# Kernel optimization log

Measured on AMD Instinct MI355X. Metric: run time of the kernel, lower is better.

Reference implementation:

```python
import jax, jax.numpy as jnp
import numpy as np

N_NODES = 100000
N_EDGES = 1600000
IN_DIM = 256
HID = 128
ALPHA = 0.1
K_STEPS = 10


def setup_inputs() -> dict:
    key = jax.random.key(0)
    ks = jax.random.split(key, 10)
    x = jax.random.normal(ks[0], (N_NODES, IN_DIM), dtype=jnp.float32)
    edge_index = jax.random.randint(ks[1], (2, N_EDGES), 0, N_NODES, dtype=jnp.int64)
    s = 0.02
    W1 = jax.random.normal(ks[2], (HID, IN_DIM), dtype=jnp.float32) * s
    b1 = jnp.zeros((HID,), dtype=jnp.float32)
    W2 = jax.random.normal(ks[3], (HID, HID), dtype=jnp.float32) * s
    b2 = jnp.zeros((HID,), dtype=jnp.float32)
    W3 = jax.random.normal(ks[4], (HID, HID), dtype=jnp.float32) * s
    b3 = jnp.zeros((HID,), dtype=jnp.float32)
    Wo = jax.random.normal(ks[5], (1, HID), dtype=jnp.float32) * s
    bo = jnp.zeros((1,), dtype=jnp.float32)
    return {"x": x, "edge_index": edge_index, "W1": W1, "b1": b1,
            "W2": W2, "b2": b2, "W3": W3, "b3": b3, "Wo": Wo, "bo": bo}


def _gcn_norm(edge_index, num_nodes):
    # add self-loops, then symmetric normalization 1/sqrt(deg_i * deg_j)
    loop = jnp.arange(num_nodes, dtype=edge_index.dtype)
    src = jnp.concatenate([edge_index[0], loop])
    dst = jnp.concatenate([edge_index[1], loop])
    ones = jnp.ones(src.shape[0], dtype=jnp.float32)
    deg = jax.ops.segment_sum(ones, dst, num_segments=num_nodes)
    dinv = jnp.where(deg > 0, jax.lax.rsqrt(deg), 0.0)
    norm = dinv[src] * dinv[dst]
    return src, dst, norm


def reference(x, edge_index, W1, b1, W2, b2, W3, b3, Wo, bo):
    # MLP encoder (dropout=0 -> identity in eval)
    h = jax.nn.relu(x @ W1.T + b1)
    h = jax.nn.relu(h @ W2.T + b2)
    h = jax.nn.relu(h @ W3.T + b3)
    # APPNP propagation: h <- (1-alpha) * A_hat h + alpha * h0
    n = x.shape[0]
    src, dst, norm = _gcn_norm(edge_index, n)
    h0 = h
    for _ in range(K_STEPS):
        msg = norm[:, None] * h[src]            # [E+N, HID]
        agg = jax.ops.segment_sum(msg, dst, num_segments=n)
        h = (1.0 - ALPHA) * agg + ALPHA * h0
    out = h @ Wo.T + bo                          # [N, 1]
    return out.squeeze(-1)
```

## Files before the change

### kernel.cpp

```cpp
#include <hip/hip_runtime.h>

#define NN   100000
#define NE   1600000
#define IND  256
#define HIDD 128
#define BCAP 64
#define NPART 196
#define SCAP 10240
#define APITCH 40
#define HPITCH 136
#define NGE  1563
#define NFA  782

typedef __attribute__((ext_vector_type(8))) short short8v;
typedef __attribute__((ext_vector_type(4))) float f32x4;

__device__ inline unsigned packbf2(float x, float y) {
  unsigned xb = __float_as_uint(x);
  unsigned yb = __float_as_uint(y);
  xb += 0x7fffu + ((xb >> 16) & 1u);
  yb += 0x7fffu + ((yb >> 16) & 1u);
  return (xb >> 16) | (yb & 0xffff0000u);
}
__device__ inline unsigned short bf16r(float x) {
  unsigned b = __float_as_uint(x);
  b += 0x7fffu + ((b >> 16) & 1u);
  return (unsigned short)(b >> 16);
}

__global__ void wcvt_all(const float* __restrict__ W1, const float* __restrict__ W2,
                         const float* __restrict__ W3, unsigned* __restrict__ W1b,
                         unsigned* __restrict__ W2b, unsigned* __restrict__ W3b) {
  int i = blockIdx.x * 256 + threadIdx.x;
  const float* src; unsigned* dst; int off;
  if (i < 16384)      { src = W1; dst = W1b; off = i; }
  else if (i < 24576) { src = W2; dst = W2b; off = i - 16384; }
  else                { src = W3; dst = W3b; off = i - 24576; }
  float2 v = ((const float2*)src)[off];
  dst[off] = packbf2(v.x, v.y);
}

__global__ __launch_bounds__(256) void enc_fillA(
    const float* __restrict__ x,
    const unsigned short* __restrict__ W1b, const float* __restrict__ b1,
    const unsigned short* __restrict__ W2b, const float* __restrict__ b2,
    const unsigned short* __restrict__ W3b, const float* __restrict__ b3,
    const float* __restrict__ Wo, float* __restrict__ z,
    const int* __restrict__ src, const int* __restrict__ dst,
    int* __restrict__ gcur, unsigned* __restrict__ sbuf)
{
  __shared__ unsigned short hbuf[64 * HPITCH];
  __shared__ float zsh[2][64];
  __shared__ int hist[NPART];
  __shared__ int lofs[NPART];
  const int tid = threadIdx.x;
  const int bid = blockIdx.x;
  const int r3v = bid % 3;

  if (r3v == 2) {
    int fi = bid / 3;
    const int base = fi * 2048;
    for (int i = tid; i < NPART; i += 256) hist[i] = 0;
    __syncthreads();
    int d[8], s[8];
#pragma unroll
    for (int i = 0; i < 8; ++i) {
      int e = base + i * 256 + tid;
      bool v = e < NE;
      d[i] = v ? dst[e] : -1;
      s[i] = v ? src[e] : 0;
      if (v) atomicAdd(&hist[d[i] >> 9], 1);
    }
    __syncthreads();
    for (int i = tid; i < NPART; i += 256)
      lofs[i] = hist[i] ? atomicAdd(&gcur[i], hist[i]) : 0;
    __syncthreads();
#pragma unroll
    for (int i = 0; i < 8; ++i) {
      if (d[i] >= 0) {
        int p = d[i] >> 9;
        int q = atomicAdd(&lofs[p], 1);
        if (q < SCAP)
          sbuf[(size_t)p * SCAP + q] = ((unsigned)(d[i] & 511) << 17) | (unsigned)s[i];
      }
    }
    return;
  }

  const int gb = (bid / 3) * 2 + r3v;
  if (gb >= NGE) return;
  unsigned short* lA = hbuf;
  const int lane = tid & 63, wid = tid >> 6;
  const int wr = wid >> 1, wc = wid & 1;
  const int bm = gb * 64;
  const int lr = lane & 15, lg = lane >> 4;

  f32x4 acc[2][4];
#pragma unroll
  for (int i = 0; i < 2; ++i)
#pragma unroll
    for (int j = 0; j < 4; ++j) acc[i][j] = (f32x4){0.f, 0.f, 0.f, 0.f};

  for (int k0 = 0; k0 < IND; k0 += 32) {
    {
      int rr = tid >> 2, g = tid & 3;
      int grow = bm + rr;
      float4 v0 = make_float4(0.f, 0.f, 0.f, 0.f), v1 = v0;
      if (grow < NN) {
        const float* ap = x + (size_t)grow * IND + k0 + g * 8;
        v0 = ((const float4*)ap)[0]; v1 = ((const float4*)ap)[1];
      }
      uint4 pk;
      pk.x = packbf2(v0.x, v0.y); pk.y = packbf2(v0.z, v0.w);
      pk.z = packbf2(v1.x, v1.y); pk.w = packbf2(v1.z, v1.w);
      *(uint4*)&lA[rr * APITCH + g * 8] = pk;
    }
    __syncthreads();
    {
      short8v a[2], b[4];
#pragma unroll
      for (int i = 0; i < 2; ++i)
        a[i] = *(const short8v*)&lA[(wr * 32 + i * 16 + lr) * APITCH + lg * 8];
#pragma unroll
      for (int j = 0; j < 4; ++j)
        b[j] = *(const short8v*)&W1b[(size_t)(wc * 64 + j * 16 + lr) * IND + k0 + lg * 8];
#pragma unroll
      for (int i = 0; i < 2; ++i)
#pragma unroll
        for (int j = 0; j < 4; ++j)
          acc[i][j] = __builtin_amdgcn_mfma_f32_16x16x32_bf16(a[i], b[j], acc[i][j], 0, 0, 0);
    }
    __syncthreads();
  }
#pragma unroll
  for (int i = 0; i < 2; ++i)
#pragma unroll
    for (int e = 0; e < 4; ++e) {
      int lrow = wr * 32 + i * 16 + lg * 4 + e;
#pragma unroll
      for (int j = 0; j < 4; ++j) {
        int cc = wc * 64 + j * 16 + lr;
        hbuf[lrow * HPITCH + cc] = bf16r(fmaxf(acc[i][j][e] + b1[cc], 0.f));
      }
    }
  __syncthreads();

#pragma unroll
  for (int i = 0; i < 2; ++i)
#pragma unroll
    for (int j = 0; j < 4; ++j) acc[i][j] = (f32x4){0.f, 0.f, 0.f, 0.f};
  for (int k0 = 0; k0 < HIDD; k0 += 32) {
    short8v a[2], b[4];
#pragma unroll
    for (int i = 0; i < 2; ++i)
      a[i] = *(const short8v*)&hbuf[(wr * 32 + i * 16 + lr) * HPITCH + k0 + lg * 8];
#pragma unroll
    for (int j = 0; j < 4; ++j)
      b[j] = *(const short8v*)&W2b[(size_t)(wc * 64 + j * 16 + lr) * HIDD + k0 + lg * 8];
#pragma unroll
    for (int i = 0; i < 2; ++i)
#pragma unroll
      for (int j = 0; j < 4; ++j)
        acc[i][j] = __builtin_amdgcn_mfma_f32_16x16x32_bf16(a[i], b[j], acc[i][j], 0, 0, 0);
  }
  __syncthreads();
#pragma unroll
  for (int i = 0; i < 2; ++i)
#pragma unroll
    for (int e = 0; e < 4; ++e) {
      int lrow = wr * 32 + i * 16 + lg * 4 + e;
#pragma unroll
      for (int j = 0; j < 4; ++j) {
        int cc = wc * 64 + j * 16 + lr;
        hbuf[lrow * HPITCH + cc] = bf16r(fmaxf(acc[i][j][e] + b2[cc], 0.f));
      }
    }
  __syncthreads();

#pragma unroll
  for (int i = 0; i < 2; ++i)
#pragma unroll
    for (int j = 0; j < 4; ++j) acc[i][j] = (f32x4){0.f, 0.f, 0.f, 0.f};
  for (int k0 = 0; k0 < HIDD; k0 += 32) {
    short8v a[2], b[4];
#pragma unroll
    for (int i = 0; i < 2; ++i)
      a[i] = *(const short8v*)&hbuf[(wr * 32 + i * 16 + lr) * HPITCH + k0 + lg * 8];
#pragma unroll
    for (int j = 0; j < 4; ++j)
      b[j] = *(const short8v*)&W3b[(size_t)(wc * 64 + j * 16 + lr) * HIDD + k0 + lg * 8];
#pragma unroll
    for (int i = 0; i < 2; ++i)
#pragma unroll
      for (int j = 0; j < 4; ++j)
        acc[i][j] = __builtin_amdgcn_mfma_f32_16x16x32_bf16(a[i], b[j], acc[i][j], 0, 0, 0);
  }
  float wv[4];
#pragma unroll
  for (int j = 0; j < 4; ++j) wv[j] = Wo[wc * 64 + j * 16 + lr];
  if (tid < 128) { zsh[tid >> 6][tid & 63] = 0.f; }
  __syncthreads();
#pragma unroll
  for (int i = 0; i < 2; ++i)
#pragma unroll
    for (int e = 0; e < 4; ++e) {
      float part = 0.f;
#pragma unroll
      for (int j = 0; j < 4; ++j) {
        int cc = wc * 64 + j * 16 + lr;
        part += fmaxf(acc[i][j][e] + b3[cc], 0.f) * wv[j];
      }
#pragma unroll
      for (int off = 8; off > 0; off >>= 1) part += __shfl_down(part, off, 16);
      if (lr == 0) zsh[wc][wr * 32 + i * 16 + lg * 4 + e] = part;
    }
  __syncthreads();
  if (tid < 64) {
    int row = bm + tid;
    if (row < NN) z[row] = zsh[0][tid] + zsh[1][tid];
  }
}

__global__ __launch_bounds__(256, 8) void fill_phaseB(
    const unsigned* __restrict__ sbuf, const int* __restrict__ gcur,
    const float* __restrict__ z, int* __restrict__ colbuk,
    int* __restrict__ deg, float* __restrict__ dinv, float* __restrict__ va)
{
  __shared__ int lcur[512];
  const int tid = threadIdx.x;
  const int b = blockIdx.x;
  for (int i = tid; i < 512; i += 256) lcur[i] = 0;
  __syncthreads();
  int cnt = min(gcur[b], SCAP);
  const unsigned* sp = sbuf + (size_t)b * SCAP;
  for (int i = tid; i < cnt; i += 256) {
    unsigned u = sp[i];
    int dloc = (int)(u >> 17);
    int s = (int)(u & 0x1FFFFu);
    int pos = atomicAdd(&lcur[dloc], 1);
    if (pos < BCAP) colbuk[(size_t)((b << 9) + dloc) * BCAP + pos] = s;
  }
  __syncthreads();
  for (int i = tid; i < 512; i += 256) {
    int node = (b << 9) + i;
    if (node < NN) {
      int dg = lcur[i];
      float di = rsqrtf((float)(dg + 1));
      deg[node] = dg;
      dinv[node] = di;
      va[node] = di * z[node];
    }
  }
}

template<int LAST>
__global__ __launch_bounds__(256, 8) void appnp_sstep(
    const float* __restrict__ vin, const float* __restrict__ z,
    const float* __restrict__ dinv, const int* __restrict__ deg,
    const int* __restrict__ colbuk, float* __restrict__ vout,
    const float* __restrict__ bo, float* __restrict__ out)
{
  int tid = threadIdx.x;
  int sl = tid & 15;
  int node = blockIdx.x * 16 + (tid >> 4);
  if (node >= NN) return;
  int m = min(deg[node], BCAP);
  float val = (sl == 0) ? vin[node] : 0.f;
  for (int j = sl; j < m; j += 16)
    val += vin[colbuk[(size_t)node * BCAP + j]];
#pragma unroll
  for (int off = 8; off > 0; off >>= 1) val += __shfl_down(val, off, 16);
  if (sl == 0) {
    float di = dinv[node];
    float s = 0.9f * di * val + 0.1f * z[node];
    if (LAST) out[node] = s + bo[0];
    else vout[node] = di * s;
  }
}

extern "C" void kernel_launch(void* const* d_in, const int* in_sizes, int n_in,
                              void* d_out, int out_size, void* d_ws, size_t ws_size,
                              hipStream_t stream) {
  const float* x   = (const float*)d_in[0];
  const int*   ei  = (const int*)d_in[1];
  const float* W1  = (const float*)d_in[2];
  const float* b1  = (const float*)d_in[3];
  const float* W2  = (const float*)d_in[4];
  const float* b2  = (const float*)d_in[5];
  const float* W3  = (const float*)d_in[6];
  const float* b3  = (const float*)d_in[7];
  const float* Wo  = (const float*)d_in[8];
  const float* bo  = (const float*)d_in[9];
  float* out = (float*)d_out;

  const int* srcv = ei;
  const int* dstv = ei + NE;

  int*      colbuk = (int*)d_ws;
  unsigned* sbuf   = (unsigned*)(colbuk + (size_t)NN * BCAP);
  int*      gcur   = (int*)(sbuf + (size_t)NPART * SCAP);
  int*      deg    = gcur + NPART;
  float*    dinv   = (float*)(deg + NN);
  float*    zbuf   = dinv + NN;
  float*    va     = zbuf + NN;
  float*    vb     = va + NN;
  unsigned* W1b    = (unsigned*)(vb + NN);
  unsigned* W2b    = W1b + 16384;
  unsigned* W3b    = W2b + 8192;

  hipMemsetAsync(gcur, 0, NPART * 4, stream);

  wcvt_all<<<128, 256, 0, stream>>>(W1, W2, W3, W1b, W2b, W3b);

  enc_fillA<<<2346, 256, 0, stream>>>(x, (unsigned short*)W1b, b1,
                                      (unsigned short*)W2b, b2,
                                      (unsigned short*)W3b, b3, Wo, zbuf,
                                      srcv, dstv, gcur, sbuf);

  fill_phaseB<<<NPART, 256, 0, stream>>>(sbuf, gcur, zbuf, colbuk, deg, dinv, va);

  int ssb = (NN + 15) / 16;
  float* cur = va; float* nxt = vb;
  for (int k = 0; k < 9; ++k) {
    appnp_sstep<0><<<ssb, 256, 0, stream>>>(cur, zbuf, dinv, deg, colbuk,
                                            nxt, nullptr, nullptr);
    float* t = cur; cur = nxt; nxt = t;
  }
  appnp_sstep<1><<<ssb, 256, 0, stream>>>(cur, zbuf, dinv, deg, colbuk,
                                          nullptr, bo, out);
}
```

Before: 207.6 us.

## Replace fixed-capacity neighbor buckets with compact CSR built via per-block scans

Measured after the change: 220.1 us. 1.06x slower.

```diff
diff --git a/kernel.cpp b/kernel.cpp
--- a/kernel.cpp
+++ b/kernel.cpp
@@ -4,13 +4,11 @@
 #define NE   1600000
 #define IND  256
 #define HIDD 128
-#define BCAP 64
 #define NPART 196
 #define SCAP 10240
 #define APITCH 40
 #define HPITCH 136
 #define NGE  1563
-#define NFA  782
 
 typedef __attribute__((ext_vector_type(8))) short short8v;
 typedef __attribute__((ext_vector_type(4))) float f32x4;
@@ -221,53 +219,91 @@
   }
 }
 
-__global__ __launch_bounds__(256, 8) void fill_phaseB(
+__global__ __launch_bounds__(256) void wscan(const int* __restrict__ gcur,
+                                             int* __restrict__ wbase) {
+  __shared__ int sc[2][256];
+  int t = threadIdx.x;
+  int v = (t < NPART) ? min(gcur[t], SCAP) : 0;
+  sc[0][t] = v;
+  __syncthreads();
+  int pp = 0;
+  for (int off = 1; off < 256; off <<= 1) {
+    sc[pp ^ 1][t] = sc[pp][t] + ((t >= off) ? sc[pp][t - off] : 0);
+    pp ^= 1;
+    __syncthreads();
+  }
+  if (t < NPART) wbase[t] = sc[pp][t] - v;
+}
+
+__global__ __launch_bounds__(256, 2) void fill_phaseB(
     const unsigned* __restrict__ sbuf, const int* __restrict__ gcur,
-    const float* __restrict__ z, int* __restrict__ colbuk,
-    int* __restrict__ deg, float* __restrict__ dinv, float* __restrict__ va)
+    const int* __restrict__ wbase, const float* __restrict__ z,
+    int* __restrict__ col, int* __restrict__ rp,
+    float* __restrict__ dinv, float* __restrict__ va)
 {
-  __shared__ int lcur[512];
+  __shared__ int lcnt[512];
+  __shared__ int sc[2][512];
+  __shared__ int excl[512];
   const int tid = threadIdx.x;
   const int b = blockIdx.x;
-  for (int i = tid; i < 512; i += 256) lcur[i] = 0;
+  lcnt[tid] = 0; lcnt[tid + 256] = 0;
   __syncthreads();
   int cnt = min(gcur[b], SCAP);
   const unsigned* sp = sbuf + (size_t)b * SCAP;
+  for (int i = tid; i < cnt; i += 256)
+    atomicAdd(&lcnt[sp[i] >> 17], 1);
+  __syncthreads();
+  sc[0][tid] = lcnt[tid]; sc[0][tid + 256] = lcnt[tid + 256];
+  __syncthreads();
+  int pp = 0;
+  for (int off = 1; off < 512; off <<= 1) {
+    int i0 = tid, i1 = tid + 256;
+    sc[pp ^ 1][i0] = sc[pp][i0] + ((i0 >= off) ? sc[pp][i0 - off] : 0);
+    sc[pp ^ 1][i1] = sc[pp][i1] + ((i1 >= off) ? sc[pp][i1 - off] : 0);
+    pp ^= 1;
+    __syncthreads();
+  }
+  const int base = wbase[b];
+#pragma unroll
+  for (int q = 0; q < 2; ++q) {
+    int i = tid + q * 256;
+    int ex = sc[pp][i] - lcnt[i];
+    excl[i] = ex;
+    int node = (b << 9) + i;
+    if (node <= NN) rp[node] = base + ex;
+    if (node < NN) {
+      float di = rsqrtf((float)(lcnt[i] + 1));
+      dinv[node] = di;
+      va[node] = di * z[node];
+    }
+  }
+  __syncthreads();
+  lcnt[tid] = 0; lcnt[tid + 256] = 0;
+  __syncthreads();
   for (int i = tid; i < cnt; i += 256) {
     unsigned u = sp[i];
-    int dloc = (int)(u >> 17);
+    int dl = (int)(u >> 17);
     int s = (int)(u & 0x1FFFFu);
-    int pos = atomicAdd(&lcur[dloc], 1);
-    if (pos < BCAP) colbuk[(size_t)((b << 9) + dloc) * BCAP + pos] = s;
-  }
-  __syncthreads();
-  for (int i = tid; i < 512; i += 256) {
-    int node = (b << 9) + i;
-    if (node < NN) {
-      int dg = lcur[i];
-      float di = rsqrtf((float)(dg + 1));
-      deg[node] = dg;
-      dinv[node] = di;
-      va[node] = di * z[node];
-    }
+    int pos = atomicAdd(&lcnt[dl], 1);
+    col[base + excl[dl] + pos] = s;
   }
 }
 
 template<int LAST>
 __global__ __launch_bounds__(256, 8) void appnp_sstep(
     const float* __restrict__ vin, const float* __restrict__ z,
-    const float* __restrict__ dinv, const int* __restrict__ deg,
-    const int* __restrict__ colbuk, float* __restrict__ vout,
+    const float* __restrict__ dinv, const int* __restrict__ rp,
+    const int* __restrict__ col, float* __restrict__ vout,
     const float* __restrict__ bo, float* __restrict__ out)
 {
   int tid = threadIdx.x;
   int sl = tid & 15;
   int node = blockIdx.x * 16 + (tid >> 4);
   if (node >= NN) return;
-  int m = min(deg[node], BCAP);
+  int beg = rp[node], end = rp[node + 1];
   float val = (sl == 0) ? vin[node] : 0.f;
-  for (int j = sl; j < m; j += 16)
-    val += vin[colbuk[(size_t)node * BCAP + j]];
+  for (int j = beg + sl; j < end; j += 16)
+    val += vin[col[j]];
 #pragma unroll
   for (int off = 8; off > 0; off >>= 1) val += __shfl_down(val, off, 16);
   if (sl == 0) {
@@ -296,11 +332,12 @@
   const int* srcv = ei;
   const int* dstv = ei + NE;
 
-  int*      colbuk = (int*)d_ws;
-  unsigned* sbuf   = (unsigned*)(colbuk + (size_t)NN * BCAP);
+  int*      col    = (int*)d_ws;
+  int*      rp     = col + NE;
+  unsigned* sbuf   = (unsigned*)(rp + NN + 1);
   int*      gcur   = (int*)(sbuf + (size_t)NPART * SCAP);
-  int*      deg    = gcur + NPART;
-  float*    dinv   = (float*)(deg + NN);
+  int*      wbase  = gcur + NPART;
+  float*    dinv   = (float*)(wbase + NPART);
   float*    zbuf   = dinv + NN;
   float*    va     = zbuf + NN;
   float*    vb     = va + NN;
@@ -317,15 +354,17 @@
                                       (unsigned short*)W3b, b3, Wo, zbuf,
                                       srcv, dstv, gcur, sbuf);
 
-  fill_phaseB<<<NPART, 256, 0, stream>>>(sbuf, gcur, zbuf, colbuk, deg, dinv, va);
+  wscan<<<1, 256, 0, stream>>>(gcur, wbase);
+  fill_phaseB<<<NPART, 256, 0, stream>>>(sbuf, gcur, wbase, zbuf,
+                                         col, rp, dinv, va);
 
   int ssb = (NN + 15) / 16;
   float* cur = va; float* nxt = vb;
   for (int k = 0; k < 9; ++k) {
-    appnp_sstep<0><<<ssb, 256, 0, stream>>>(cur, zbuf, dinv, deg, colbuk,
+    appnp_sstep<0><<<ssb, 256, 0, stream>>>(cur, zbuf, dinv, rp, col,
                                             nxt, nullptr, nullptr);
     float* t = cur; cur = nxt; nxt = t;
   }
-  appnp_sstep<1><<<ssb, 256, 0, stream>>>(cur, zbuf, dinv, deg, colbuk,
+  appnp_sstep<1><<<ssb, 256, 0, stream>>>(cur, zbuf, dinv, rp, col,
                                           nullptr, bo, out);
 }
```
